# Kernel optimization log

Hardware: AMD Instinct MI355X
Metric: run time of the kernel (lower is better)

The kernel has to match this reference:

```python
import jax, jax.numpy as jnp
import numpy as np

B, IN, D, L = 512, 512, 64, 256
WF = 0.5  # writter_f = 1.0 * w_0


def setup_inputs() -> dict:
    key = jax.random.key(0)
    ks = jax.random.split(key, 12)
    u = lambda i, s: jax.random.uniform(ks[i], s, jnp.float32, -0.05, 0.05)
    return {
        "x": jax.random.normal(ks[0], (B, IN), jnp.float32),
        "memory": u(1, (L, L)),
        "kernel_1": u(2, (IN, 60)), "bias_1": jnp.zeros((1, 60), jnp.float32),
        "kernel_2_0": u(3, (60, 50)), "bias_2_0": jnp.zeros((1, 50), jnp.float32),
        "kernel_3_0": u(4, (60, 50)), "bias_3_0": jnp.zeros((1, 50), jnp.float32),
        "kernel_4_0": u(5, (60, 50)), "bias_4_0": jnp.zeros((1, 50), jnp.float32),
        "kernel_2": u(6, (50, D)), "bias_2": jnp.zeros((1, D), jnp.float32),
        "kernel_3": u(7, (50, D)), "bias_3": jnp.zeros((1, D), jnp.float32),
        "kernel_4": u(8, (50, L)), "bias_4": jnp.zeros((1, L), jnp.float32),
        "kernel_r": u(9, (L, D, L)),
        "kernel_w": u(10, (L, D, L)),
        "w_sig": u(11, (L * L, 1)),
    }


def reference(x, memory, kernel_1, bias_1, kernel_2_0, bias_2_0, kernel_3_0,
              bias_3_0, kernel_4_0, bias_4_0, kernel_2, bias_2, kernel_3,
              bias_3, kernel_4, bias_4, kernel_r, kernel_w, w_sig):
    b = x.shape[0]
    l1 = jax.nn.relu(x @ kernel_1 + bias_1)                                  # (B, 60)
    # write path
    lfw = jax.nn.relu(jax.nn.relu(l1 @ kernel_3_0 + bias_3_0) @ kernel_3 + bias_3)  # (B, D)
    lbw = jnp.tanh(jax.nn.relu(l1 @ kernel_4_0 + bias_4_0) @ kernel_4 + bias_4)     # (B, L)
    lw = jax.nn.softmax(jnp.einsum('bd,jdl->jbl', lfw, kernel_w), axis=-1)   # (L, B, L)
    # wj = memory[j] * lwj * (1 + wf * lbw[j]); note lbw[j] indexes BATCH row j
    w = memory[:, None, :] * lw * (1.0 + WF * lbw[:L, None, :])              # (L, B, L)
    mem_new = w.reshape(L * b, L)                                            # concat over j on axis 0
    # read path (uses only first L rows of the updated memory)
    lf = jax.nn.relu(jax.nn.relu(l1 @ kernel_2_0 + bias_2_0) @ kernel_2 + bias_2)   # (B, D)
    lr = jax.nn.softmax(jnp.einsum('bd,idl->ibl', lf, kernel_r), axis=-1)    # (L, B, L)
    readed = (mem_new[:L][:, None, :] * lr).transpose(1, 0, 2).reshape(b, L * L)
    return jax.nn.sigmoid(readed @ w_sig)                                    # (B, 1)
```

## Files before the change

kernel.cpp:

```cpp
#include <hip/hip_runtime.h>
#include <hip/hip_bf16.h>
#include <math.h>


typedef __attribute__((ext_vector_type(8))) short short8;
typedef __attribute__((ext_vector_type(4))) float f32x4;

static __device__ __forceinline__ unsigned short f2bf(float f) {
    __hip_bfloat16 h = __float2bfloat16(f);
    return *reinterpret_cast<unsigned short*>(&h);
}

__global__ __launch_bounds__(256) void k_front(
    const float* __restrict__ x,
    const float* __restrict__ k1,  const float* __restrict__ b1,
    const float* __restrict__ k20, const float* __restrict__ b20,
    const float* __restrict__ k2,  const float* __restrict__ b2,
    const float* __restrict__ k30, const float* __restrict__ b30,
    const float* __restrict__ k3,  const float* __restrict__ b3,
    const float* __restrict__ k40, const float* __restrict__ b40,
    const float* __restrict__ k4,  const float* __restrict__ b4,
    unsigned short* __restrict__ lf_bf,
    float* __restrict__ lfw,
    float* __restrict__ lbw0) {
    __shared__ float xs[512];
    __shared__ float part[4][64];
    __shared__ float l1s[60];
    __shared__ float hid2[50], hid3[50], hid4[50];
    const int b = blockIdx.x, t = threadIdx.x;
    const int c = t & 63, kq = t >> 6;

    {
        const float2 xv = *(const float2*)&x[b * 512 + t * 2];
        xs[t * 2] = xv.x;
        xs[t * 2 + 1] = xv.y;
    }
    __syncthreads();

    {
        float a0 = 0.f, a1 = 0.f, a2 = 0.f, a3 = 0.f;
        float a4 = 0.f, a5 = 0.f, a6 = 0.f, a7 = 0.f;
        if (c < 60) {
            const float* xk = xs + kq * 128;
            const float* kp = k1 + (kq * 128) * 60 + c;
#pragma unroll 2
            for (int k = 0; k < 128; k += 8) {
                a0 += xk[k + 0] * kp[(k + 0) * 60];
                a1 += xk[k + 1] * kp[(k + 1) * 60];
                a2 += xk[k + 2] * kp[(k + 2) * 60];
                a3 += xk[k + 3] * kp[(k + 3) * 60];
                a4 += xk[k + 4] * kp[(k + 4) * 60];
                a5 += xk[k + 5] * kp[(k + 5) * 60];
                a6 += xk[k + 6] * kp[(k + 6) * 60];
                a7 += xk[k + 7] * kp[(k + 7) * 60];
            }
        }
        part[kq][c] = ((a0 + a1) + (a2 + a3)) + ((a4 + a5) + (a6 + a7));
    }
    __syncthreads();
    if (t < 60)
        l1s[t] = fmaxf(b1[t] + part[0][t] + part[1][t] + part[2][t] + part[3][t], 0.f);
    __syncthreads();

    if (t < 50) {
        float a = b20[t];
#pragma unroll
        for (int k = 0; k < 60; ++k) a += l1s[k] * k20[k * 50 + t];
        hid2[t] = fmaxf(a, 0.f);
    } else if (t >= 64 && t < 114 && b < 256) {
        const int j = t - 64;
        float a = b30[j];
#pragma unroll
        for (int k = 0; k < 60; ++k) a += l1s[k] * k30[k * 50 + j];
        hid3[j] = fmaxf(a, 0.f);
    } else if (t >= 128 && t < 178 && b == 0) {
        const int j = t - 128;
        float a = b40[j];
#pragma unroll
        for (int k = 0; k < 60; ++k) a += l1s[k] * k40[k * 50 + j];
        hid4[j] = fmaxf(a, 0.f);
    }
    __syncthreads();

    if (t < 64) {
        float a = b2[t];
#pragma unroll
        for (int k = 0; k < 50; ++k) a += hid2[k] * k2[k * 64 + t];
        lf_bf[b * 64 + t] = f2bf(fmaxf(a, 0.f));
    } else if (t < 128 && b < 256) {
        const int j = t - 64;
        float a = b3[j];
#pragma unroll
        for (int k = 0; k < 50; ++k) a += hid3[k] * k3[k * 64 + j];
        lfw[b * 64 + j] = fmaxf(a, 0.f);
    }
    if (b == 0) {
        __syncthreads();
        float a = b4[t];
#pragma unroll
        for (int k = 0; k < 50; ++k) a += hid4[k] * k4[k * 256 + t];
        lbw0[t] = tanhf(a);
    }
}

__global__ __launch_bounds__(512, 1) void k_mainc(
    const unsigned short* __restrict__ lf,
    const float* __restrict__ kernel_r,
    const float* __restrict__ lfw,
    const float* __restrict__ kw,
    const float* __restrict__ mem,
    const float* __restrict__ lbw0,
    const float* __restrict__ wsig,
    float* __restrict__ partial) {
    __shared__ __align__(16) unsigned short KrT[256 * 64];
    __shared__ float cLDS[256];
    __shared__ float wpart[4];
    const int i = blockIdx.x;
    const int tid = threadIdx.x;
    const int lane = tid & 63;
    const int wv = tid >> 6;

    {
        const int l = tid & 255;
        const int dh = tid >> 8;
        const float* src = kernel_r + (size_t)i * 16384 + (size_t)dh * 32 * 256 + l;
        float v[32];
#pragma unroll
        for (int j = 0; j < 32; ++j) v[j] = src[(size_t)j * 256];
        char* lds = (char*)KrT;
#pragma unroll
        for (int j = 0; j < 16; ++j) {
            const int d = dh * 32 + 2 * j;
            const unsigned int pk =
                (unsigned int)f2bf(v[2 * j]) | ((unsigned int)f2bf(v[2 * j + 1]) << 16);
            const int byteoff = ((l * 64 + d) * 2) ^ ((l & 7) << 4);
            *(unsigned int*)(lds + byteoff) = pk;
        }
    }

    float e_c = 0.f, cf = 0.f;
    if (tid < 256) {
        const int l = tid;
        cf = mem[l] * (1.f + 0.5f * lbw0[l]) * wsig[i * 256 + l];
        float s0 = 0.f, s1 = 0.f, s2 = 0.f, s3 = 0.f;
        const float* lrow = lfw + i * 64;
        const float* kp = kw + l;
#pragma unroll 4
        for (int d = 0; d < 64; d += 4) {
            s0 += lrow[d + 0] * kp[(d + 0) * 256];
            s1 += lrow[d + 1] * kp[(d + 1) * 256];
            s2 += lrow[d + 2] * kp[(d + 2) * 256];
            s3 += lrow[d + 3] * kp[(d + 3) * 256];
        }
        e_c = __expf((s0 + s1) + (s2 + s3));
        float se = e_c;
#pragma unroll
        for (int off = 1; off < 64; off <<= 1) se += __shfl_xor(se, off, 64);
        if (lane == 0) wpart[wv] = se;
    }
    __syncthreads();
    if (tid < 256) {
        const float tot = wpart[0] + wpart[1] + wpart[2] + wpart[3];
        cLDS[tid] = cf * (e_c / tot);
    }
    __syncthreads();

    const int c = lane & 15, g = lane >> 4;

    short8 Af0[4], Af1[4];
#pragma unroll
    for (int p = 0; p < 4; ++p) {
        const int b0 = wv * 64 + p * 16;
        Af0[p] = *(const short8*)(lf + (b0 + c) * 64 + g * 8);
        Af1[p] = *(const short8*)(lf + (b0 + c) * 64 + 32 + g * 8);
    }

    short8 Bf0[16], Bf1[16];
    {
        const char* lds = (const char*)KrT;
#pragma unroll
        for (int n = 0; n < 16; ++n) {
            const int l = n * 16 + c;
            const int base = l * 128 + g * 16;
            Bf0[n] = *(const short8*)(lds + ((base) ^ ((l & 7) << 4)));
            Bf1[n] = *(const short8*)(lds + ((base + 64) ^ ((l & 7) << 4)));
        }
    }
    float ccv[16];
#pragma unroll
    for (int n = 0; n < 16; ++n) ccv[n] = cLDS[n * 16 + c];

#pragma unroll
    for (int p = 0; p < 4; ++p) {
        const int b0 = wv * 64 + p * 16;
        f32x4 acc[16];
#pragma unroll
        for (int n = 0; n < 16; ++n) acc[n] = (f32x4){0.f, 0.f, 0.f, 0.f};
#pragma unroll
        for (int n = 0; n < 16; ++n) {
            acc[n] = __builtin_amdgcn_mfma_f32_16x16x32_bf16(Af0[p], Bf0[n], acc[n], 0, 0, 0);
            acc[n] = __builtin_amdgcn_mfma_f32_16x16x32_bf16(Af1[p], Bf1[n], acc[n], 0, 0, 0);
        }
#pragma unroll
        for (int r = 0; r < 4; ++r) {
            float se = 0.f, sw = 0.f;
#pragma unroll
            for (int n = 0; n < 16; ++n) {
                const float e = __expf(acc[n][r]);
                se += e;
                sw += ccv[n] * e;
            }
#pragma unroll
            for (int off = 1; off < 16; off <<= 1) {
                se += __shfl_xor(se, off, 64);
                sw += __shfl_xor(sw, off, 64);
            }
            if (c == 0) partial[(b0 + g * 4 + r) * 256 + i] = sw / se;
        }
    }
}

__global__ __launch_bounds__(256) void k_out2(const float* __restrict__ partial,
                                              float* __restrict__ out) {
    const int t = threadIdx.x;
    const int rq = t >> 6, lane = t & 63;
    const int row = blockIdx.x * 4 + rq;
    const f32x4 v = *(const f32x4*)&partial[row * 256 + lane * 4];
    float s = v.x + v.y + v.z + v.w;
#pragma unroll
    for (int off = 1; off < 64; off <<= 1) s += __shfl_xor(s, off, 64);
    if (lane == 0) out[row] = 1.f / (1.f + __expf(-s));
}

extern "C" void kernel_launch(void* const* d_in, const int* in_sizes, int n_in,
                              void* d_out, int out_size, void* d_ws, size_t ws_size,
                              hipStream_t stream) {
    (void)in_sizes; (void)n_in; (void)out_size; (void)ws_size;
    const float* x    = (const float*)d_in[0];
    const float* mem  = (const float*)d_in[1];
    const float* k1   = (const float*)d_in[2];
    const float* b1   = (const float*)d_in[3];
    const float* k20  = (const float*)d_in[4];
    const float* b20  = (const float*)d_in[5];
    const float* k30  = (const float*)d_in[6];
    const float* b30  = (const float*)d_in[7];
    const float* k40  = (const float*)d_in[8];
    const float* b40  = (const float*)d_in[9];
    const float* k2   = (const float*)d_in[10];
    const float* b2   = (const float*)d_in[11];
    const float* k3   = (const float*)d_in[12];
    const float* b3   = (const float*)d_in[13];
    const float* k4   = (const float*)d_in[14];
    const float* b4   = (const float*)d_in[15];
    const float* kr   = (const float*)d_in[16];
    const float* kw   = (const float*)d_in[17];
    const float* wsig = (const float*)d_in[18];
    float* out = (float*)d_out;

    float* ws   = (float*)d_ws;
    float* lfw  = ws;
    float* lbw0 = lfw + 256 * 64;
    float* part = lbw0 + 256;
    unsigned short* lf_bf = (unsigned short*)(part + 131072);

    hipLaunchKernelGGL(k_front, dim3(512), dim3(256), 0, stream, x,
                       k1, b1, k20, b20, k2, b2, k30, b30, k3, b3,
                       k40, b40, k4, b4, lf_bf, lfw, lbw0);
    hipLaunchKernelGGL(k_mainc, dim3(256), dim3(512), 0, stream,
                       lf_bf, kr, lfw, kw, mem, lbw0, wsig, part);
    hipLaunchKernelGGL(k_out2,  dim3(128), dim3(256), 0, stream, part, out);
}
```

Before: 29.07 us.

## Prescale Kr by log2e for exp2, vectorize LDS stores, split front-end accumulators

Kernel_r values are multiplied by log2(e) before the bf16 conversion, so the softmax exponent can use exp2f directly and skip a multiply per element. The LDS transpose-store loop now packs values and writes 16-byte vector stores instead of 4-byte stores, keeping the XOR swizzle on 16-byte granules. The small dense layers in the front kernel use several independent accumulators to shorten the FMA dependency chains. Scaling before bf16 rounding changes the rounding slightly, and vector stores could cause LDS bank conflicts.

Measured after the change: 33.04 us. +13.7%, slower.

```diff
diff --git a/kernel.cpp b/kernel.cpp
--- a/kernel.cpp
+++ b/kernel.cpp
@@ -5,6 +5,9 @@
 
 typedef __attribute__((ext_vector_type(8))) short short8;
 typedef __attribute__((ext_vector_type(4))) float f32x4;
+typedef __attribute__((ext_vector_type(4))) unsigned int u32x4;
+
+#define LOG2E 1.44269504088896340736f
 
 static __device__ __forceinline__ unsigned short f2bf(float f) {
     __hip_bfloat16 h = __float2bfloat16(f);
@@ -63,16 +66,26 @@
     __syncthreads();
 
     if (t < 50) {
-        float a = b20[t];
-#pragma unroll
-        for (int k = 0; k < 60; ++k) a += l1s[k] * k20[k * 50 + t];
-        hid2[t] = fmaxf(a, 0.f);
+        float a0 = b20[t], a1 = 0.f, a2 = 0.f, a3 = 0.f;
+#pragma unroll
+        for (int k = 0; k < 60; k += 4) {
+            a0 += l1s[k + 0] * k20[(k + 0) * 50 + t];
+            a1 += l1s[k + 1] * k20[(k + 1) * 50 + t];
+            a2 += l1s[k + 2] * k20[(k + 2) * 50 + t];
+            a3 += l1s[k + 3] * k20[(k + 3) * 50 + t];
+        }
+        hid2[t] = fmaxf((a0 + a1) + (a2 + a3), 0.f);
     } else if (t >= 64 && t < 114 && b < 256) {
         const int j = t - 64;
-        float a = b30[j];
-#pragma unroll
-        for (int k = 0; k < 60; ++k) a += l1s[k] * k30[k * 50 + j];
-        hid3[j] = fmaxf(a, 0.f);
+        float a0 = b30[j], a1 = 0.f, a2 = 0.f, a3 = 0.f;
+#pragma unroll
+        for (int k = 0; k < 60; k += 4) {
+            a0 += l1s[k + 0] * k30[(k + 0) * 50 + j];
+            a1 += l1s[k + 1] * k30[(k + 1) * 50 + j];
+            a2 += l1s[k + 2] * k30[(k + 2) * 50 + j];
+            a3 += l1s[k + 3] * k30[(k + 3) * 50 + j];
+        }
+        hid3[j] = fmaxf((a0 + a1) + (a2 + a3), 0.f);
     } else if (t >= 128 && t < 178 && b == 0) {
         const int j = t - 128;
         float a = b40[j];
@@ -83,16 +96,22 @@
     __syncthreads();
 
     if (t < 64) {
-        float a = b2[t];
-#pragma unroll
-        for (int k = 0; k < 50; ++k) a += hid2[k] * k2[k * 64 + t];
-        lf_bf[b * 64 + t] = f2bf(fmaxf(a, 0.f));
+        float a0 = b2[t], a1 = 0.f;
+#pragma unroll
+        for (int k = 0; k < 50; k += 2) {
+            a0 += hid2[k + 0] * k2[(k + 0) * 64 + t];
+            a1 += hid2[k + 1] * k2[(k + 1) * 64 + t];
+        }
+        lf_bf[b * 64 + t] = f2bf(fmaxf(a0 + a1, 0.f));
     } else if (t < 128 && b < 256) {
         const int j = t - 64;
-        float a = b3[j];
-#pragma unroll
-        for (int k = 0; k < 50; ++k) a += hid3[k] * k3[k * 64 + j];
-        lfw[b * 64 + j] = fmaxf(a, 0.f);
+        float a0 = b3[j], a1 = 0.f;
+#pragma unroll
+        for (int k = 0; k < 50; k += 2) {
+            a0 += hid3[k + 0] * k3[(k + 0) * 64 + j];
+            a1 += hid3[k + 1] * k3[(k + 1) * 64 + j];
+        }
+        lfw[b * 64 + j] = fmaxf(a0 + a1, 0.f);
     }
     if (b == 0) {
         __syncthreads();
@@ -127,14 +146,18 @@
         float v[32];
 #pragma unroll
         for (int j = 0; j < 32; ++j) v[j] = src[(size_t)j * 256];
+        unsigned int pk[16];
+#pragma unroll
+        for (int j = 0; j < 16; ++j)
+            pk[j] = (unsigned int)f2bf(v[2 * j] * LOG2E) |
+                    ((unsigned int)f2bf(v[2 * j + 1] * LOG2E) << 16);
         char* lds = (char*)KrT;
-#pragma unroll
-        for (int j = 0; j < 16; ++j) {
-            const int d = dh * 32 + 2 * j;
-            const unsigned int pk =
-                (unsigned int)f2bf(v[2 * j]) | ((unsigned int)f2bf(v[2 * j + 1]) << 16);
-            const int byteoff = ((l * 64 + d) * 2) ^ ((l & 7) << 4);
-            *(unsigned int*)(lds + byteoff) = pk;
+        const int rowbase = l * 128 + dh * 64;
+#pragma unroll
+        for (int q = 0; q < 4; ++q) {
+            const int byteoff = (rowbase + q * 16) ^ ((l & 7) << 4);
+            *(u32x4*)(lds + byteoff) =
+                (u32x4){pk[4 * q], pk[4 * q + 1], pk[4 * q + 2], pk[4 * q + 3]};
         }
     }
 
@@ -206,7 +229,7 @@
             float se = 0.f, sw = 0.f;
 #pragma unroll
             for (int n = 0; n < 16; ++n) {
-                const float e = __expf(acc[n][r]);
+                const float e = exp2f(acc[n][r]);
                 se += e;
                 sw += ccv[n] * e;
             }
```
